# Optimization experiments

Measured on AMD Instinct MI355X. Metric: run time of the kernel, lower is better.

Reference implementation:

```python
import jax, jax.numpy as jnp
import numpy as np

EPS = 1e-5

def grid_sample_bilinear(img, grid):
    """torch F.grid_sample, mode='bilinear', padding_mode='zeros', align_corners=True.
    img: (b, c, H, W); grid: (b, Hg, Wg, 2) with (x, y) in [-1, 1]. Returns (b, c, Hg, Wg)."""
    H, W = img.shape[2], img.shape[3]
    x = (grid[..., 0] + 1.0) * 0.5 * (W - 1)
    y = (grid[..., 1] + 1.0) * 0.5 * (H - 1)
    x0 = jnp.floor(x); y0 = jnp.floor(y)
    x1 = x0 + 1.0;     y1 = y0 + 1.0
    wx1 = x - x0; wx0 = 1.0 - wx1
    wy1 = y - y0; wy0 = 1.0 - wy1

    def sample_one(img_b, yi, xi):
        # img_b: (c,H,W); yi, xi: (Hg,Wg) float corner coords
        valid = ((yi >= 0) & (yi < H) & (xi >= 0) & (xi < W)).astype(img_b.dtype)
        yc = jnp.clip(yi, 0, H - 1).astype(jnp.int32)
        xc = jnp.clip(xi, 0, W - 1).astype(jnp.int32)
        return img_b[:, yc, xc] * valid[None]  # (c,Hg,Wg)

    def per_batch(img_b, x0b, x1b, y0b, y1b, wx0b, wx1b, wy0b, wy1b):
        v = (sample_one(img_b, y0b, x0b) * (wy0b * wx0b)[None]
             + sample_one(img_b, y0b, x1b) * (wy0b * wx1b)[None]
             + sample_one(img_b, y1b, x0b) * (wy1b * wx0b)[None]
             + sample_one(img_b, y1b, x1b) * (wy1b * wx1b)[None])
        return v

    return jax.vmap(per_batch)(img, x0, x1, y0, y1, wx0, wx1, wy0, wy1)


def conv_bn_relu(x, w, gamma, beta):
    # 1x1 conv (no bias) + BatchNorm2d (batch stats, training-mode forward) + ReLU
    y = jnp.einsum('nchw,oc->nohw', x, w)
    mean = y.mean(axis=(0, 2, 3), keepdims=True)
    var = y.var(axis=(0, 2, 3), keepdims=True)
    y = (y - mean) * jax.lax.rsqrt(var + EPS)
    y = y * gamma[None, :, None, None] + beta[None, :, None, None]
    return jax.nn.relu(y)


def setup_inputs() -> dict:
    key = jax.random.key(0)
    ks = jax.random.split(key, 10)
    b, c, h, w, r = 1, 128, 64, 128, 4
    d = 2 * r + 1
    f1 = jax.random.normal(ks[0], (b, c, h, w), dtype=jnp.float32)
    f2 = jax.random.normal(ks[1], (b, c, h, w), dtype=jnp.float32)
    # coords: base pixel grid (x, y) plus a small random flow perturbation
    gy, gx = jnp.meshgrid(jnp.arange(h, dtype=jnp.float32), jnp.arange(w, dtype=jnp.float32), indexing='ij')
    base = jnp.stack([gx, gy], axis=0)[None]  # (1,2,h,w)
    coords = base + 2.0 * jax.random.normal(ks[2], (b, 2, h, w), dtype=jnp.float32)
    c1, c2, c3 = 96, 128, 64
    w1 = jax.random.normal(ks[3], (c1, 2 * c), dtype=jnp.float32) * 0.05
    w2 = jax.random.normal(ks[4], (c2, c1), dtype=jnp.float32) * 0.05
    w3 = jax.random.normal(ks[5], (c3, c2), dtype=jnp.float32) * 0.05
    w4 = jax.random.normal(ks[6], (1, c3), dtype=jnp.float32) * 0.05
    b4 = jnp.zeros((1,), dtype=jnp.float32)
    g1 = jnp.ones((c1,), jnp.float32); be1 = jnp.zeros((c1,), jnp.float32)
    g2 = jnp.ones((c2,), jnp.float32); be2 = jnp.zeros((c2,), jnp.float32)
    g3 = jnp.ones((c3,), jnp.float32); be3 = jnp.zeros((c3,), jnp.float32)
    # DAP: identity init + small noise so gradients are non-trivial
    wdap = jnp.eye(d * d, dtype=jnp.float32) + 0.01 * jax.random.normal(ks[7], (d * d, d * d), dtype=jnp.float32)
    return {"f1": f1, "f2": f2, "coords": coords,
            "w1": w1, "g1": g1, "be1": be1,
            "w2": w2, "g2": g2, "be2": be2,
            "w3": w3, "g3": g3, "be3": be3,
            "w4": w4, "b4": b4, "wdap": wdap, "radius": 4}


def reference(f1, f2, coords, w1, g1, be1, w2, g2, be2, w3, g3, be3, w4, b4, wdap, radius):
    b, c, h, w = f1.shape
    r = radius
    d = 2 * r + 1
    dx = jnp.linspace(-r, r, d, dtype=f1.dtype)
    delta = jnp.stack(jnp.meshgrid(dx, dx, indexing='ij'), axis=-1)  # (d,d,2)
    coords_p = jnp.transpose(coords, (0, 2, 3, 1))  # (b,h,w,2)
    cent = coords_p[:, None, :, None, :, :] + delta.reshape(1, d, 1, d, 1, 2)  # (b,d,h,d,w,2)
    cx = 2.0 * cent[..., 0] / (w - 1) - 1.0
    cy = 2.0 * cent[..., 1] / (h - 1) - 1.0
    grid = jnp.stack([cx, cy], axis=-1).reshape(b, d * h, d * w, 2)
    f2s = grid_sample_bilinear(f2, grid)                     # (b,c,d*h,d*w)
    f2s = f2s.reshape(b, c, d, h, d, w).transpose(0, 2, 4, 1, 3, 5)  # (b,d,d,c,h,w)
    f1e = jnp.broadcast_to(f1[:, None, None], (b, d, d, c, h, w))
    corr = jnp.concatenate([f1e, f2s], axis=3).reshape(b * d * d, 2 * c, h, w)
    x = conv_bn_relu(corr, w1, g1, be1)
    x = conv_bn_relu(x, w2, g2, be2)
    x = conv_bn_relu(x, w3, g3, be3)
    cost = jnp.einsum('nchw,oc->nohw', x, w4) + b4[None, :, None, None]  # (b*d*d,1,h,w)
    cost = cost.reshape(b, d * d, h, w)
    # DAP: 1x1 conv over the d*d displacement channels, no bias
    cost = jnp.einsum('bkhw,lk->blhw', cost, wdap)
    return cost  # (b, (2r+1)^2, h, w)
```

## Files before the change

kernel.cpp:

```cpp
#include <hip/hip_runtime.h>
#include <hip/hip_bf16.h>

#define H 64
#define W 128
#define P 8192
#define DD 81
#define NS 663552
#define C1 96
#define C2 128
#define C3 64
#define EPSF 1e-5f
#define NSLOT 128

#define X1S 104
#define X2S 136
#define Y3S 72
#define X1TS 136

#define NGB 648

typedef __attribute__((ext_vector_type(8))) short bf16x8;
typedef __attribute__((ext_vector_type(4))) float f32x4;

#define S1SUM 0
#define S1SSQ (S1SUM + NSLOT * C1)
#define M1SUM (S1SSQ + NSLOT * C1)
#define GOFF  (M1SUM + NSLOT * C2)
#define S3SUM (GOFF + NSLOT * C2)
#define S3SSQ (S3SUM + NSLOT * C3)
#define STATS_ZERO_FLOATS (S3SSQ + NSLOT * C3)
#define S1Sc 73728
#define S1Tc (S1Sc + C1)
#define S2Sc (S1Tc + C1)
#define S2Tc (S2Sc + C2)
#define S3Sc (S2Tc + C2)
#define S3Tc (S3Sc + C3)
#define COST_OFF 74304
#define FLOAT_END (COST_OFF + NS)
#define A_BYTE   ((size_t)FLOAT_END * 4)
#define G_BYTE   (A_BYTE + (size_t)P * 96 * 2)
#define W2BF_BYTE (G_BYTE + (size_t)P * 96 * 2)
#define W3BF_BYTE (W2BF_BYTE + (size_t)C2 * C1 * 2)
#define Y1_BYTE  (W3BF_BYTE + (size_t)C3 * C2 * 2)
#define Y3_BYTE  (Y1_BYTE + (size_t)NS * C1 * 2)
#define WS_NEEDED (Y3_BYTE + (size_t)NS * C3 * 2)
#define GPART_BYTE Y3_BYTE

__device__ __forceinline__ float bflo(unsigned u) { return __uint_as_float(u << 16); }
__device__ __forceinline__ float bfhi(unsigned u) { return __uint_as_float(u & 0xffff0000u); }
__device__ __forceinline__ float bfu(unsigned short v) { return __uint_as_float((unsigned)v << 16); }

__device__ __forceinline__ unsigned pkbf(float a, float b) {
  __hip_bfloat162 h = __float22bfloat162_rn(make_float2(a, b));
  unsigned u; __builtin_memcpy(&u, &h, 4);
  return u;
}

__global__ __launch_bounds__(256) void k_prep(const float* __restrict__ f1,
                                              const float* __restrict__ f2,
                                              const float* __restrict__ w1,
                                              unsigned short* __restrict__ aT,
                                              unsigned short* __restrict__ gT) {
  __shared__ float tile[128][64];
  int t = threadIdx.x;
  int p0 = blockIdx.x * 64;
  int px = t & 63, q = t >> 6;
  int c0 = q * 24;
  for (int pass = 0; pass < 2; ++pass) {
    const float* src = pass ? f2 : f1;
    unsigned short* dst = pass ? gT : aT;
    int koff = pass ? 128 : 0;
    __syncthreads();
    for (int idx = t; idx < 8192; idx += 256) {
      int kk = idx >> 6, xx = idx & 63;
      tile[kk][xx] = src[kk * P + p0 + xx];
    }
    __syncthreads();
    float acc[24];
#pragma unroll
    for (int i = 0; i < 24; ++i) acc[i] = 0.f;
    for (int kk = 0; kk < 128; ++kk) {
      float fv = tile[kk][px];
#pragma unroll
      for (int i = 0; i < 24; ++i)
        acc[i] += w1[(c0 + i) * 256 + koff + kk] * fv;
    }
#pragma unroll
    for (int i = 0; i < 24; i += 4) {
      uint2 pk;
      pk.x = pkbf(acc[i + 0], acc[i + 1]);
      pk.y = pkbf(acc[i + 2], acc[i + 3]);
      *(uint2*)(dst + ((size_t)((c0 + i) >> 2) * P + p0 + px) * 4) = pk;
    }
  }
}

__global__ void k_wprep(const float* __restrict__ w2, const float* __restrict__ w3,
                        unsigned short* __restrict__ w2bf, unsigned short* __restrict__ w3bf) {
  int idx = blockIdx.x * 256 + threadIdx.x;
  if (idx < C2 * C1) {
    w2bf[idx] = (unsigned short)(pkbf(w2[idx], 0.f) & 0xffffu);
  } else if (idx < C2 * C1 + C3 * C2) {
    w3bf[idx - C2 * C1] = (unsigned short)(pkbf(w3[idx - C2 * C1], 0.f) & 0xffffu);
  }
}

__global__ __launch_bounds__(256) void k_sample(const float* __restrict__ coords,
                                                float* __restrict__ ws,
                                                const unsigned short* __restrict__ aT,
                                                const unsigned short* __restrict__ gT,
                                                unsigned short* __restrict__ y1T) {
  int t = threadIdx.x, b = blockIdx.x;
  int cg = b % 6;
  int ptile = b / 6;
  int c = cg * 4 + (t >> 6);
  int px = t & 63;
  int p = ptile * 64 + px;
  float cx = coords[p], cy = coords[P + p];
  float fx0 = floorf(cx), fy0 = floorf(cy);
  float wx1 = cx - fx0, wx0 = 1.f - wx1;
  float wy1 = cy - fy0, wy0 = 1.f - wy1;
  int ixb = (int)fx0 - 4, iyb = (int)fy0 - 4;
  int colOff[10];
  float vx[10];
#pragma unroll
  for (int j = 0; j < 10; ++j) {
    int ix = ixb + j;
    vx[j] = (ix >= 0 && ix < W) ? 1.f : 0.f;
    colOff[j] = min(max(ix, 0), W - 1);
  }
  float ewx0[9], ewx1[9];
#pragma unroll
  for (int j = 0; j < 9; ++j) { ewx0[j] = wx0 * vx[j]; ewx1[j] = wx1 * vx[j + 1]; }
  int rowOff[10];
  float vy[10];
#pragma unroll
  for (int dy = 0; dy < 10; ++dy) {
    int iy = iyb + dy;
    vy[dy] = (iy >= 0 && iy < H) ? 1.f : 0.f;
    rowOff[dy] = min(max(iy, 0), H - 1) * W;
  }
  float ewy0[9], ewy1[9];
#pragma unroll
  for (int d = 0; d < 9; ++d) { ewy0[d] = wy0 * vy[d]; ewy1[d] = wy1 * vy[d + 1]; }
  float av[4];
  {
    uint2 a2 = *(const uint2*)(aT + ((size_t)c * P + p) * 4);
    av[0] = bflo(a2.x); av[1] = bfhi(a2.x); av[2] = bflo(a2.y); av[3] = bfhi(a2.y);
  }
  const unsigned short* gc = gT + (size_t)c * P * 4;
  float Hb[2][9][4];
  float sum[4] = {0.f, 0.f, 0.f, 0.f}, ssq[4] = {0.f, 0.f, 0.f, 0.f};
#pragma unroll
  for (int dy = 0; dy < 10; ++dy) {
    const int cur = dy & 1, prv = cur ^ 1;
    uint2 gv[10];
    const unsigned short* grow = gc + (size_t)rowOff[dy] * 4;
#pragma unroll
    for (int j = 0; j < 10; ++j) gv[j] = *(const uint2*)(grow + colOff[j] * 4);
#pragma unroll
    for (int j = 0; j < 9; ++j) {
      Hb[cur][j][0] = fmaf(ewx1[j], bflo(gv[j + 1].x), ewx0[j] * bflo(gv[j].x));
      Hb[cur][j][1] = fmaf(ewx1[j], bfhi(gv[j + 1].x), ewx0[j] * bfhi(gv[j].x));
      Hb[cur][j][2] = fmaf(ewx1[j], bflo(gv[j + 1].y), ewx0[j] * bflo(gv[j].y));
      Hb[cur][j][3] = fmaf(ewx1[j], bfhi(gv[j + 1].y), ewx0[j] * bfhi(gv[j].y));
    }
    if (dy >= 1) {
      const int dyk = dy - 1;
      float e0 = ewy0[dyk], e1 = ewy1[dyk];
#pragma unroll
      for (int j = 0; j < 9; ++j) {
        float o0 = fmaf(e0, Hb[prv][j][0], fmaf(e1, Hb[cur][j][0], av[0]));
        float o1 = fmaf(e0, Hb[prv][j][1], fmaf(e1, Hb[cur][j][1], av[1]));
        float o2 = fmaf(e0, Hb[prv][j][2], fmaf(e1, Hb[cur][j][2], av[2]));
        float o3 = fmaf(e0, Hb[prv][j][3], fmaf(e1, Hb[cur][j][3], av[3]));
        sum[0] += o0; ssq[0] = fmaf(o0, o0, ssq[0]);
        sum[1] += o1; ssq[1] = fmaf(o1, o1, ssq[1]);
        sum[2] += o2; ssq[2] = fmaf(o2, o2, ssq[2]);
        sum[3] += o3; ssq[3] = fmaf(o3, o3, ssq[3]);
        uint2 pk;
        pk.x = pkbf(o0, o1);
        pk.y = pkbf(o2, o3);
        int kk = j * 9 + dyk;
        *(uint2*)(y1T + (((size_t)kk * 24 + c) * P + p) * 4) = pk;
      }
    }
  }
#pragma unroll
  for (int m = 1; m < 64; m <<= 1) {
#pragma unroll
    for (int e = 0; e < 4; ++e) {
      sum[e] += __shfl_xor(sum[e], m);
      ssq[e] += __shfl_xor(ssq[e], m);
    }
  }
  if ((t & 63) == 0) {
    int slot = b & (NSLOT - 1);
#pragma unroll
    for (int e = 0; e < 4; ++e) {
      atomicAdd(&ws[S1SUM + slot * C1 + c * 4 + e], sum[e]);
      atomicAdd(&ws[S1SSQ + slot * C1 + c * 4 + e], ssq[e]);
    }
  }
}

__global__ void k_finalize(float* __restrict__ ws, int sumO, int ssqO,
                           const float* __restrict__ gamma, const float* __restrict__ beta,
                           int sO, int tO, int C) {
  int c = threadIdx.x;
  if (c < C) {
    float su = 0.f, sq = 0.f;
    for (int s = 0; s < NSLOT; ++s) { su += ws[sumO + s * C + c]; sq += ws[ssqO + s * C + c]; }
    float mean = su * (1.0f / (float)NS);
    float var = sq * (1.0f / (float)NS) - mean * mean;
    float sc = gamma[c] * rsqrtf(var + EPSF);
    ws[sO + c] = sc;
    ws[tO + c] = beta[c] - mean * sc;
  }
}

__global__ __launch_bounds__(256) void k_gram(const unsigned short* __restrict__ y1T,
                                              float* __restrict__ ws,
                                              float* __restrict__ gpart) {
  __shared__ unsigned short x1t[96 * X1TS];
  int t = threadIdx.x, b = blockIdx.x;
  int w = t >> 6, l = t & 63;
  int lr = l & 15, lh = l >> 4;
  int i0 = (w >> 1) * 48, j0 = (w & 1) * 48;
  f32x4 acc[9];
  f32x4 zero4 = {0.f, 0.f, 0.f, 0.f};
#pragma unroll
  for (int q = 0; q < 9; ++q) acc[q] = zero4;
  int c = t >> 3, pg = t & 7;
  float s1v[4], t1v[4];
  if (c < 24) {
#pragma unroll
    for (int e = 0; e < 4; ++e) { s1v[e] = ws[S1Sc + c * 4 + e]; t1v[e] = ws[S1Tc + c * 4 + e]; }
  }
  float msum[4] = {0.f, 0.f, 0.f, 0.f};
  for (int it = 0; it < 8; ++it) {
    int idx = b * 8 + it;
    int k = idx >> 6, p0 = (idx & 63) << 7;
    const unsigned short* y1k = y1T + (size_t)k * P * 96;
    __syncthreads();
    if (c < 24) {
      int pbase = p0 + pg * 16;
      unsigned rowu[4][8];
#pragma unroll
      for (int ii = 0; ii < 8; ++ii) {
        uint4 v = *(const uint4*)(y1k + ((size_t)c * P + pbase + ii * 2) * 4);
        float x00 = fmaxf(0.f, fmaf(s1v[0], bflo(v.x), t1v[0]));
        float x10 = fmaxf(0.f, fmaf(s1v[1], bfhi(v.x), t1v[1]));
        float x20 = fmaxf(0.f, fmaf(s1v[2], bflo(v.y), t1v[2]));
        float x30 = fmaxf(0.f, fmaf(s1v[3], bfhi(v.y), t1v[3]));
        float x01 = fmaxf(0.f, fmaf(s1v[0], bflo(v.z), t1v[0]));
        float x11 = fmaxf(0.f, fmaf(s1v[1], bfhi(v.z), t1v[1]));
        float x21 = fmaxf(0.f, fmaf(s1v[2], bflo(v.w), t1v[2]));
        float x31 = fmaxf(0.f, fmaf(s1v[3], bfhi(v.w), t1v[3]));
        msum[0] += x00 + x01; msum[1] += x10 + x11;
        msum[2] += x20 + x21; msum[3] += x30 + x31;
        rowu[0][ii] = pkbf(x00, x01);
        rowu[1][ii] = pkbf(x10, x11);
        rowu[2][ii] = pkbf(x20, x21);
        rowu[3][ii] = pkbf(x30, x31);
      }
#pragma unroll
      for (int e = 0; e < 4; ++e) {
        unsigned short* dst = x1t + (c * 4 + e) * X1TS + pg * 16;
        uint4 pk0; pk0.x = rowu[e][0]; pk0.y = rowu[e][1]; pk0.z = rowu[e][2]; pk0.w = rowu[e][3];
        uint4 pk1; pk1.x = rowu[e][4]; pk1.y = rowu[e][5]; pk1.z = rowu[e][6]; pk1.w = rowu[e][7];
        *(uint4*)dst = pk0;
        *(uint4*)(dst + 8) = pk1;
      }
    }
    __syncthreads();
#pragma unroll
    for (int kk = 0; kk < 4; ++kk) {
      bf16x8 a3[3], b3[3];
#pragma unroll
      for (int a = 0; a < 3; ++a)
        a3[a] = *(const bf16x8*)(const void*)(x1t + (i0 + a * 16 + lr) * X1TS + kk * 32 + lh * 8);
#pragma unroll
      for (int bb = 0; bb < 3; ++bb)
        b3[bb] = *(const bf16x8*)(const void*)(x1t + (j0 + bb * 16 + lr) * X1TS + kk * 32 + lh * 8);
#pragma unroll
      for (int a = 0; a < 3; ++a)
#pragma unroll
        for (int bb = 0; bb < 3; ++bb)
          acc[a * 3 + bb] = __builtin_amdgcn_mfma_f32_16x16x32_bf16(a3[a], b3[bb], acc[a * 3 + bb], 0, 0, 0);
    }
  }
  {
    float* gp = gpart + (size_t)b * 9216;
#pragma unroll
    for (int a = 0; a < 3; ++a)
#pragma unroll
      for (int bb = 0; bb < 3; ++bb) {
        int ti = (w >> 1) * 3 + a, tj = (w & 1) * 3 + bb;
        f32x4 v = acc[a * 3 + bb];
#pragma unroll
        for (int r = 0; r < 4; ++r)
          gp[(ti * 16 + lh * 4 + r) * 96 + tj * 16 + lr] = v[r];
      }
  }
  if (c < 24) {
#pragma unroll
    for (int m = 1; m < 8; m <<= 1)
#pragma unroll
      for (int e = 0; e < 4; ++e) msum[e] += __shfl_xor(msum[e], m);
    if (pg == 0) {
      int slot = b & (NSLOT - 1);
#pragma unroll
      for (int e = 0; e < 4; ++e) atomicAdd(&ws[M1SUM + slot * 96 + c * 4 + e], msum[e]);
    }
  }
}

__global__ void k_greduce(const float* __restrict__ gpart, float* __restrict__ ws) {
  int e = blockIdx.x * 256 + threadIdx.x;
  float s = 0.f;
  for (int b = 0; b < NGB; ++b) s += gpart[(size_t)b * 9216 + e];
  ws[GOFF + e] = s;
}

__global__ __launch_bounds__(256) void k_fin2g(float* __restrict__ ws,
                                               const unsigned short* __restrict__ w2bf,
                                               const float* __restrict__ g2,
                                               const float* __restrict__ be2) {
  __shared__ float wrow[96];
  __shared__ float m1f[96];
  __shared__ float red[8];
  int o = blockIdx.x, t = threadIdx.x;
  if (t < 96) {
    wrow[t] = bfu(w2bf[o * 96 + t]);
    float s = 0.f;
    for (int sl = 0; sl < NSLOT; ++sl) s += ws[M1SUM + sl * 96 + t];
    m1f[t] = s;
  }
  __syncthreads();
  float quad = 0.f;
  for (int e = t; e < 9216; e += 256) {
    int i = e / 96, j = e - i * 96;
    quad = fmaf(wrow[i] * wrow[j], ws[GOFF + e], quad);
  }
  float msm = (t < 96) ? wrow[t] * m1f[t] : 0.f;
#pragma unroll
  for (int m = 1; m < 64; m <<= 1) { quad += __shfl_xor(quad, m); msm += __shfl_xor(msm, m); }
  if ((t & 63) == 0) { red[t >> 6] = quad; red[4 + (t >> 6)] = msm; }
  __syncthreads();
  if (t == 0) {
    float q = red[0] + red[1] + red[2] + red[3];
    float mm = red[4] + red[5] + red[6] + red[7];
    float mean = mm * (1.0f / (float)NS);
    float var = q * (1.0f / (float)NS) - mean * mean;
    float sc = g2[o] * rsqrtf(var + EPSF);
    ws[S2Sc + o] = sc;
    ws[S2Tc + o] = be2[o] - mean * sc;
  }
}

__device__ __forceinline__ void build_x1(const unsigned short* __restrict__ y1k,
                                         const float* __restrict__ ws,
                                         unsigned short* lds, int p0, int t) {
  int s = t >> 1, hh = t & 1;
  int p = p0 + s;
  const float* s1p = ws + S1Sc;
  const float* t1p = ws + S1Tc;
  unsigned short* base = lds + s * X1S + hh * 48;
#pragma unroll
  for (int i2 = 0; i2 < 6; ++i2) {
    int c0 = hh * 12 + i2 * 2;
    uint2 va = *(const uint2*)(y1k + ((size_t)c0 * P + p) * 4);
    uint2 vb = *(const uint2*)(y1k + ((size_t)(c0 + 1) * P + p) * 4);
    int cb = c0 * 4;
    float x0 = fmaxf(0.f, fmaf(s1p[cb + 0], bflo(va.x), t1p[cb + 0]));
    float x1 = fmaxf(0.f, fmaf(s1p[cb + 1], bfhi(va.x), t1p[cb + 1]));
    float x2 = fmaxf(0.f, fmaf(s1p[cb + 2], bflo(va.y), t1p[cb + 2]));
    float x3 = fmaxf(0.f, fmaf(s1p[cb + 3], bfhi(va.y), t1p[cb + 3]));
    float x4 = fmaxf(0.f, fmaf(s1p[cb + 4], bflo(vb.x), t1p[cb + 4]));
    float x5 = fmaxf(0.f, fmaf(s1p[cb + 5], bfhi(vb.x), t1p[cb + 5]));
    float x6 = fmaxf(0.f, fmaf(s1p[cb + 6], bflo(vb.y), t1p[cb + 6]));
    float x7 = fmaxf(0.f, fmaf(s1p[cb + 7], bfhi(vb.y), t1p[cb + 7]));
    uint4 pk;
    pk.x = pkbf(x0, x1); pk.y = pkbf(x2, x3); pk.z = pkbf(x4, x5); pk.w = pkbf(x6, x7);
    *(uint4*)(base + i2 * 8) = pk;
  }
}

__global__ __launch_bounds__(256) void k_l23(const unsigned short* __restrict__ y1T,
                                             float* __restrict__ ws,
                                             const unsigned short* __restrict__ w2bf,
                                             const unsigned short* __restrict__ w3bf,
                                             unsigned short* __restrict__ y3) {
  __shared__ unsigned short ldss[128 * X1S];
  int t = threadIdx.x, b = blockIdx.x;
  int k = b >> 6, p0 = (b & 63) << 7;
  size_t n0 = (size_t)k * P + p0;
  int slot = b & (NSLOT - 1);
  const unsigned short* y1k = y1T + (size_t)k * P * 96;
  build_x1(y1k, ws, ldss, p0, t);
  __syncthreads();
  int l = t & 63, wv = t >> 6;
  int o0w = wv * 32;
  int lr = l & 15, lh = l >> 4;
  bf16x8 af[2][3];
#pragma unroll
  for (int m = 0; m < 2; ++m)
#pragma unroll
    for (int kk = 0; kk < 3; ++kk)
      af[m][kk] = *(const bf16x8*)(const void*)(w2bf + (size_t)(o0w + m * 16 + lr) * 96 + kk * 32 + lh * 8);
  f32x4 acc[2][8];
  f32x4 zero4 = {0.f, 0.f, 0.f, 0.f};
#pragma unroll
  for (int m = 0; m < 2; ++m)
#pragma unroll
    for (int n = 0; n < 8; ++n) acc[m][n] = zero4;
#pragma unroll
  for (int kk = 0; kk < 3; ++kk)
#pragma unroll
    for (int n = 0; n < 8; ++n) {
      bf16x8 bfr = *(const bf16x8*)(const void*)(ldss + (n * 16 + lr) * X1S + kk * 32 + lh * 8);
      acc[0][n] = __builtin_amdgcn_mfma_f32_16x16x32_bf16(af[0][kk], bfr, acc[0][n], 0, 0, 0);
      acc[1][n] = __builtin_amdgcn_mfma_f32_16x16x32_bf16(af[1][kk], bfr, acc[1][n], 0, 0, 0);
    }
  float s2v[2][4], t2v[2][4];
#pragma unroll
  for (int m = 0; m < 2; ++m)
#pragma unroll
    for (int r = 0; r < 4; ++r) {
      int cc = o0w + m * 16 + lh * 4 + r;
      s2v[m][r] = ws[S2Sc + cc];
      t2v[m][r] = ws[S2Tc + cc];
    }
  int o2 = wv * 16;
  bf16x8 af2[4];
#pragma unroll
  for (int kk = 0; kk < 4; ++kk)
    af2[kk] = *(const bf16x8*)(const void*)(w3bf + (size_t)(o2 + lr) * 128 + kk * 32 + lh * 8);
  unsigned short* x2s = ldss;
  unsigned short* y3a = ldss + 8704;
  float ssum[4] = {0.f, 0.f, 0.f, 0.f}, sssq[4] = {0.f, 0.f, 0.f, 0.f};
#pragma unroll
  for (int h = 0; h < 2; ++h) {
    __syncthreads();
#pragma unroll
    for (int m = 0; m < 2; ++m)
#pragma unroll
      for (int n2 = 0; n2 < 4; ++n2) {
        f32x4 v = acc[m][h * 4 + n2];
        float x0 = fmaxf(0.f, fmaf(s2v[m][0], v[0], t2v[m][0]));
        float x1v = fmaxf(0.f, fmaf(s2v[m][1], v[1], t2v[m][1]));
        float x2v = fmaxf(0.f, fmaf(s2v[m][2], v[2], t2v[m][2]));
        float x3 = fmaxf(0.f, fmaf(s2v[m][3], v[3], t2v[m][3]));
        uint2 pk;
        pk.x = pkbf(x0, x1v);
        pk.y = pkbf(x2v, x3);
        *(uint2*)(x2s + (n2 * 16 + lr) * X2S + o0w + m * 16 + lh * 4) = pk;
      }
    __syncthreads();
    f32x4 acc2[4];
#pragma unroll
    for (int n2 = 0; n2 < 4; ++n2) acc2[n2] = zero4;
#pragma unroll
    for (int kk = 0; kk < 4; ++kk)
#pragma unroll
      for (int n2 = 0; n2 < 4; ++n2) {
        bf16x8 bfr = *(const bf16x8*)(const void*)(x2s + (n2 * 16 + lr) * X2S + kk * 32 + lh * 8);
        acc2[n2] = __builtin_amdgcn_mfma_f32_16x16x32_bf16(af2[kk], bfr, acc2[n2], 0, 0, 0);
      }
#pragma unroll
    for (int n2 = 0; n2 < 4; ++n2) {
      f32x4 v = acc2[n2];
#pragma unroll
      for (int r = 0; r < 4; ++r) { float x = v[r]; ssum[r] += x; sssq[r] = fmaf(x, x, sssq[r]); }
    }
    __syncthreads();
    unsigned short* dst = h ? ldss : y3a;
#pragma unroll
    for (int n2 = 0; n2 < 4; ++n2) {
      f32x4 v = acc2[n2];
      uint2 pk;
      pk.x = pkbf(v[0], v[1]);
      pk.y = pkbf(v[2], v[3]);
      *(uint2*)(dst + (n2 * 16 + lr) * Y3S + o2 + lh * 4) = pk;
    }
  }
#pragma unroll
  for (int msk = 1; msk < 16; msk <<= 1)
#pragma unroll
    for (int i = 0; i < 4; ++i) { ssum[i] += __shfl_xor(ssum[i], msk); sssq[i] += __shfl_xor(sssq[i], msk); }
  if (lr == 0) {
#pragma unroll
    for (int r = 0; r < 4; ++r) {
      int o = o2 + lh * 4 + r;
      atomicAdd(&ws[S3SUM + slot * C3 + o], ssum[r]);
      atomicAdd(&ws[S3SSQ + slot * C3 + o], sssq[r]);
    }
  }
  __syncthreads();
  {
    int row = t >> 1, hf = t & 1;
    const unsigned short* src = (row < 64) ? (y3a + row * Y3S) : (ldss + (row - 64) * Y3S);
    const uint4* s4 = (const uint4*)(src + hf * 32);
    uint4* dst = (uint4*)(y3 + (n0 + row) * 64 + hf * 32);
#pragma unroll
    for (int j = 0; j < 4; ++j) dst[j] = s4[j];
  }
}

__global__ __launch_bounds__(256) void k_layer4(const unsigned short* __restrict__ y3,
                                                float* __restrict__ ws,
                                                const float* __restrict__ w4,
                                                const float* __restrict__ b4) {
  int n = blockIdx.x * 256 + threadIdx.x;
  const float* s3p = ws + S3Sc;
  const float* t3p = ws + S3Tc;
  const uint4* row = (const uint4*)(y3 + (size_t)n * C3);
  float acc = 0.f;
#pragma unroll
  for (int j = 0; j < 8; ++j) {
    uint4 v = row[j];
    unsigned arr[4] = {v.x, v.y, v.z, v.w};
#pragma unroll
    for (int e = 0; e < 4; ++e) {
      int c = j * 8 + e * 2;
      acc += fmaxf(0.f, fmaf(s3p[c], bflo(arr[e]), t3p[c])) * w4[c];
      acc += fmaxf(0.f, fmaf(s3p[c + 1], bfhi(arr[e]), t3p[c + 1])) * w4[c + 1];
    }
  }
  ws[COST_OFF + n] = acc + b4[0];
}

__global__ __launch_bounds__(256) void k_dap(const float* __restrict__ ws,
                                             const float* __restrict__ wdap,
                                             float* __restrict__ out) {
  __shared__ float wd[DD * DD];
  int t = threadIdx.x;
  for (int i = t; i < DD * DD; i += 256) wd[i] = wdap[i];
  __syncthreads();
  int p = blockIdx.x * 32 + (t & 31);
  int lg = t >> 5;
  const float* cost = ws + COST_OFF;
  float cr[81];
#pragma unroll
  for (int kk = 0; kk < 81; ++kk) cr[kk] = cost[kk * P + p];
  for (int l = lg; l < 81; l += 8) {
    float acc = 0.f;
#pragma unroll
    for (int kk = 0; kk < 81; ++kk) acc = fmaf(wd[l * 81 + kk], cr[kk], acc);
    out[(size_t)l * P + p] = acc;
  }
}

__global__ void k_marker(float* out) { out[0] = 1.0e30f; }

extern "C" void kernel_launch(void* const* d_in, const int* in_sizes, int n_in,
                              void* d_out, int out_size, void* d_ws, size_t ws_size,
                              hipStream_t stream) {
  const float* f1 = (const float*)d_in[0];
  const float* f2 = (const float*)d_in[1];
  const float* coords = (const float*)d_in[2];
  const float* w1 = (const float*)d_in[3];
  const float* g1 = (const float*)d_in[4];
  const float* be1 = (const float*)d_in[5];
  const float* w2 = (const float*)d_in[6];
  const float* g2 = (const float*)d_in[7];
  const float* be2 = (const float*)d_in[8];
  const float* w3 = (const float*)d_in[9];
  const float* g3 = (const float*)d_in[10];
  const float* be3 = (const float*)d_in[11];
  const float* w4 = (const float*)d_in[12];
  const float* b4 = (const float*)d_in[13];
  const float* wdap = (const float*)d_in[14];
  float* out = (float*)d_out;
  float* ws = (float*)d_ws;

  if (ws_size < WS_NEEDED) {
    k_marker<<<1, 1, 0, stream>>>(out);
    return;
  }
  unsigned short* aT = (unsigned short*)((char*)d_ws + A_BYTE);
  unsigned short* gT = (unsigned short*)((char*)d_ws + G_BYTE);
  unsigned short* w2bf = (unsigned short*)((char*)d_ws + W2BF_BYTE);
  unsigned short* w3bf = (unsigned short*)((char*)d_ws + W3BF_BYTE);
  unsigned short* y1T = (unsigned short*)((char*)d_ws + Y1_BYTE);
  unsigned short* y3 = (unsigned short*)((char*)d_ws + Y3_BYTE);
  float* gpart = (float*)((char*)d_ws + GPART_BYTE);

  hipMemsetAsync(d_ws, 0, (size_t)STATS_ZERO_FLOATS * 4, stream);
  k_prep<<<128, 256, 0, stream>>>(f1, f2, w1, aT, gT);
  k_wprep<<<80, 256, 0, stream>>>(w2, w3, w2bf, w3bf);
  k_sample<<<768, 256, 0, stream>>>(coords, ws, aT, gT, y1T);
  k_finalize<<<1, 128, 0, stream>>>(ws, S1SUM, S1SSQ, g1, be1, S1Sc, S1Tc, C1);
  k_gram<<<NGB, 256, 0, stream>>>(y1T, ws, gpart);
  k_greduce<<<36, 256, 0, stream>>>(gpart, ws);
  k_fin2g<<<128, 256, 0, stream>>>(ws, w2bf, g2, be2);
  k_l23<<<5184, 256, 0, stream>>>(y1T, ws, w2bf, w3bf, y3);
  k_finalize<<<1, 128, 0, stream>>>(ws, S3SUM, S3SSQ, g3, be3, S3Sc, S3Tc, C3);
  k_layer4<<<2592, 256, 0, stream>>>(y3, ws, w4, b4);
  k_dap<<<256, 256, 0, stream>>>(ws, wdap, out);
}
```

Baseline: 329.1 us.

## Store layer-3 output channel-blocked and reduce Gram partials via atomic slots

Layer-3 activations are now written straight from registers in a channel-group-major layout (4 channels per group), so the LDS staging, the extra barriers and the row copy-out in k_l23 go away. k_layer4 reads this layout with coalesced 8-byte loads across threads. Separately, k_gram now uses half as many blocks, each covering twice the work, and accumulates its 96x96 partial Gram into 8 atomic slots instead of writing 648 full partials, which shrinks the k_greduce pass. The cost is atomic contention on the slots, a larger memset of the stats region, and narrower 8-byte global stores from k_l23.

```diff
diff --git a/kernel.cpp b/kernel.cpp
--- a/kernel.cpp
+++ b/kernel.cpp
@@ -14,10 +14,10 @@
 
 #define X1S 104
 #define X2S 136
-#define Y3S 72
 #define X1TS 136
 
-#define NGB 648
+#define NGB 324
+#define NGSLOT 8
 
 typedef __attribute__((ext_vector_type(8))) short bf16x8;
 typedef __attribute__((ext_vector_type(4))) float f32x4;
@@ -25,17 +25,18 @@
 #define S1SUM 0
 #define S1SSQ (S1SUM + NSLOT * C1)
 #define M1SUM (S1SSQ + NSLOT * C1)
-#define GOFF  (M1SUM + NSLOT * C2)
-#define S3SUM (GOFF + NSLOT * C2)
+#define S3SUM (M1SUM + NSLOT * C1)
 #define S3SSQ (S3SUM + NSLOT * C3)
-#define STATS_ZERO_FLOATS (S3SSQ + NSLOT * C3)
-#define S1Sc 73728
+#define GSLOT (S3SSQ + NSLOT * C3)
+#define STATS_ZERO_FLOATS (GSLOT + NGSLOT * 9216)
+#define S1Sc 126976
 #define S1Tc (S1Sc + C1)
 #define S2Sc (S1Tc + C1)
 #define S2Tc (S2Sc + C2)
 #define S3Sc (S2Tc + C2)
 #define S3Tc (S3Sc + C3)
-#define COST_OFF 74304
+#define GOFF 127552
+#define COST_OFF (GOFF + 9216)
 #define FLOAT_END (COST_OFF + NS)
 #define A_BYTE   ((size_t)FLOAT_END * 4)
 #define G_BYTE   (A_BYTE + (size_t)P * 96 * 2)
@@ -44,7 +45,6 @@
 #define Y1_BYTE  (W3BF_BYTE + (size_t)C3 * C2 * 2)
 #define Y3_BYTE  (Y1_BYTE + (size_t)NS * C1 * 2)
 #define WS_NEEDED (Y3_BYTE + (size_t)NS * C3 * 2)
-#define GPART_BYTE Y3_BYTE
 
 __device__ __forceinline__ float bflo(unsigned u) { return __uint_as_float(u << 16); }
 __device__ __forceinline__ float bfhi(unsigned u) { return __uint_as_float(u & 0xffff0000u); }
@@ -220,8 +220,7 @@
 }
 
 __global__ __launch_bounds__(256) void k_gram(const unsigned short* __restrict__ y1T,
-                                              float* __restrict__ ws,
-                                              float* __restrict__ gpart) {
+                                              float* __restrict__ ws) {
   __shared__ unsigned short x1t[96 * X1TS];
   int t = threadIdx.x, b = blockIdx.x;
   int w = t >> 6, l = t & 63;
@@ -238,8 +237,8 @@
     for (int e = 0; e < 4; ++e) { s1v[e] = ws[S1Sc + c * 4 + e]; t1v[e] = ws[S1Tc + c * 4 + e]; }
   }
   float msum[4] = {0.f, 0.f, 0.f, 0.f};
-  for (int it = 0; it < 8; ++it) {
-    int idx = b * 8 + it;
+  for (int it = 0; it < 16; ++it) {
+    int idx = b * 16 + it;
     int k = idx >> 6, p0 = (idx & 63) << 7;
     const unsigned short* y1k = y1T + (size_t)k * P * 96;
     __syncthreads();
@@ -291,7 +290,7 @@
     }
   }
   {
-    float* gp = gpart + (size_t)b * 9216;
+    float* gp = ws + GSLOT + (b & (NGSLOT - 1)) * 9216;
 #pragma unroll
     for (int a = 0; a < 3; ++a)
 #pragma unroll
@@ -300,7 +299,7 @@
         f32x4 v = acc[a * 3 + bb];
 #pragma unroll
         for (int r = 0; r < 4; ++r)
-          gp[(ti * 16 + lh * 4 + r) * 96 + tj * 16 + lr] = v[r];
+          atomicAdd(&gp[(ti * 16 + lh * 4 + r) * 96 + tj * 16 + lr], v[r]);
       }
   }
   if (c < 24) {
@@ -311,15 +310,16 @@
     if (pg == 0) {
       int slot = b & (NSLOT - 1);
 #pragma unroll
-      for (int e = 0; e < 4; ++e) atomicAdd(&ws[M1SUM + slot * 96 + c * 4 + e], msum[e]);
-    }
-  }
-}
-
-__global__ void k_greduce(const float* __restrict__ gpart, float* __restrict__ ws) {
+      for (int e = 0; e < 4; ++e) atomicAdd(&ws[M1SUM + slot * C1 + c * 4 + e], msum[e]);
+    }
+  }
+}
+
+__global__ void k_greduce(float* __restrict__ ws) {
   int e = blockIdx.x * 256 + threadIdx.x;
   float s = 0.f;
-  for (int b = 0; b < NGB; ++b) s += gpart[(size_t)b * 9216 + e];
+#pragma unroll
+  for (int g = 0; g < NGSLOT; ++g) s += ws[GSLOT + g * 9216 + e];
   ws[GOFF + e] = s;
 }
 
@@ -334,7 +334,7 @@
   if (t < 96) {
     wrow[t] = bfu(w2bf[o * 96 + t]);
     float s = 0.f;
-    for (int sl = 0; sl < NSLOT; ++sl) s += ws[M1SUM + sl * 96 + t];
+    for (int sl = 0; sl < NSLOT; ++sl) s += ws[M1SUM + sl * C1 + t];
     m1f[t] = s;
   }
   __syncthreads();
@@ -391,7 +391,7 @@
                                              float* __restrict__ ws,
                                              const unsigned short* __restrict__ w2bf,
                                              const unsigned short* __restrict__ w3bf,
-                                             unsigned short* __restrict__ y3) {
+                                             unsigned short* __restrict__ y3T) {
   __shared__ unsigned short ldss[128 * X1S];
   int t = threadIdx.x, b = blockIdx.x;
   int k = b >> 6, p0 = (b & 63) << 7;
@@ -433,12 +433,12 @@
       t2v[m][r] = ws[S2Tc + cc];
     }
   int o2 = wv * 16;
+  int ch4 = wv * 4 + lh;
   bf16x8 af2[4];
 #pragma unroll
   for (int kk = 0; kk < 4; ++kk)
     af2[kk] = *(const bf16x8*)(const void*)(w3bf + (size_t)(o2 + lr) * 128 + kk * 32 + lh * 8);
   unsigned short* x2s = ldss;
-  unsigned short* y3a = ldss + 8704;
   float ssum[4] = {0.f, 0.f, 0.f, 0.f}, sssq[4] = {0.f, 0.f, 0.f, 0.f};
 #pragma unroll
   for (int h = 0; h < 2; ++h) {
@@ -473,16 +473,11 @@
       f32x4 v = acc2[n2];
 #pragma unroll
       for (int r = 0; r < 4; ++r) { float x = v[r]; ssum[r] += x; sssq[r] = fmaf(x, x, sssq[r]); }
-    }
-    __syncthreads();
-    unsigned short* dst = h ? ldss : y3a;
-#pragma unroll
-    for (int n2 = 0; n2 < 4; ++n2) {
-      f32x4 v = acc2[n2];
       uint2 pk;
       pk.x = pkbf(v[0], v[1]);
       pk.y = pkbf(v[2], v[3]);
-      *(uint2*)(dst + (n2 * 16 + lr) * Y3S + o2 + lh * 4) = pk;
+      size_t n = n0 + h * 64 + n2 * 16 + lr;
+      *(uint2*)(y3T + ((size_t)ch4 * NS + n) * 4) = pk;
     }
   }
 #pragma unroll
@@ -497,36 +492,24 @@
       atomicAdd(&ws[S3SSQ + slot * C3 + o], sssq[r]);
     }
   }
-  __syncthreads();
-  {
-    int row = t >> 1, hf = t & 1;
-    const unsigned short* src = (row < 64) ? (y3a + row * Y3S) : (ldss + (row - 64) * Y3S);
-    const uint4* s4 = (const uint4*)(src + hf * 32);
-    uint4* dst = (uint4*)(y3 + (n0 + row) * 64 + hf * 32);
-#pragma unroll
-    for (int j = 0; j < 4; ++j) dst[j] = s4[j];
-  }
-}
-
-__global__ __launch_bounds__(256) void k_layer4(const unsigned short* __restrict__ y3,
+}
+
+__global__ __launch_bounds__(256) void k_layer4(const unsigned short* __restrict__ y3T,
                                                 float* __restrict__ ws,
                                                 const float* __restrict__ w4,
                                                 const float* __restrict__ b4) {
-  int n = blockIdx.x * 256 + threadIdx.x;
+  size_t n = (size_t)blockIdx.x * 256 + threadIdx.x;
   const float* s3p = ws + S3Sc;
   const float* t3p = ws + S3Tc;
-  const uint4* row = (const uint4*)(y3 + (size_t)n * C3);
   float acc = 0.f;
 #pragma unroll
-  for (int j = 0; j < 8; ++j) {
-    uint4 v = row[j];
-    unsigned arr[4] = {v.x, v.y, v.z, v.w};
-#pragma unroll
-    for (int e = 0; e < 4; ++e) {
-      int c = j * 8 + e * 2;
-      acc += fmaxf(0.f, fmaf(s3p[c], bflo(arr[e]), t3p[c])) * w4[c];
-      acc += fmaxf(0.f, fmaf(s3p[c + 1], bfhi(arr[e]), t3p[c + 1])) * w4[c + 1];
-    }
+  for (int c16 = 0; c16 < 16; ++c16) {
+    uint2 v = *(const uint2*)(y3T + ((size_t)c16 * NS + n) * 4);
+    int c = c16 * 4;
+    acc += fmaxf(0.f, fmaf(s3p[c + 0], bflo(v.x), t3p[c + 0])) * w4[c + 0];
+    acc += fmaxf(0.f, fmaf(s3p[c + 1], bfhi(v.x), t3p[c + 1])) * w4[c + 1];
+    acc += fmaxf(0.f, fmaf(s3p[c + 2], bflo(v.y), t3p[c + 2])) * w4[c + 2];
+    acc += fmaxf(0.f, fmaf(s3p[c + 3], bfhi(v.y), t3p[c + 3])) * w4[c + 3];
   }
   ws[COST_OFF + n] = acc + b4[0];
 }
@@ -584,19 +567,18 @@
   unsigned short* w2bf = (unsigned short*)((char*)d_ws + W2BF_BYTE);
   unsigned short* w3bf = (unsigned short*)((char*)d_ws + W3BF_BYTE);
   unsigned short* y1T = (unsigned short*)((char*)d_ws + Y1_BYTE);
-  unsigned short* y3 = (unsigned short*)((char*)d_ws + Y3_BYTE);
-  float* gpart = (float*)((char*)d_ws + GPART_BYTE);
+  unsigned short* y3T = (unsigned short*)((char*)d_ws + Y3_BYTE);
 
   hipMemsetAsync(d_ws, 0, (size_t)STATS_ZERO_FLOATS * 4, stream);
   k_prep<<<128, 256, 0, stream>>>(f1, f2, w1, aT, gT);
   k_wprep<<<80, 256, 0, stream>>>(w2, w3, w2bf, w3bf);
   k_sample<<<768, 256, 0, stream>>>(coords, ws, aT, gT, y1T);
   k_finalize<<<1, 128, 0, stream>>>(ws, S1SUM, S1SSQ, g1, be1, S1Sc, S1Tc, C1);
-  k_gram<<<NGB, 256, 0, stream>>>(y1T, ws, gpart);
-  k_greduce<<<36, 256, 0, stream>>>(gpart, ws);
+  k_gram<<<NGB, 256, 0, stream>>>(y1T, ws);
+  k_greduce<<<36, 256, 0, stream>>>(ws);
   k_fin2g<<<128, 256, 0, stream>>>(ws, w2bf, g2, be2);
-  k_l23<<<5184, 256, 0, stream>>>(y1T, ws, w2bf, w3bf, y3);
+  k_l23<<<5184, 256, 0, stream>>>(y1T, ws, w2bf, w3bf, y3T);
   k_finalize<<<1, 128, 0, stream>>>(ws, S3SUM, S3SSQ, g3, be3, S3Sc, S3Tc, C3);
-  k_layer4<<<2592, 256, 0, stream>>>(y3, ws, w4, b4);
+  k_layer4<<<2592, 256, 0, stream>>>(y3T, ws, w4, b4);
   k_dap<<<256, 256, 0, stream>>>(ws, wdap, out);
 }
```

Result: faster. 294.1 us (-10.6%).
